# Kernel tuning notes

Measured on AMD Instinct MI355X. Metric: run time of the kernel, lower is better.

Reference implementation:

```python
import jax, jax.numpy as jnp
import numpy as np

B, S = 8, 512
HIDDEN = 513
SPATIAL = HIDDEN - 1           # 512
F = SPATIAL // 2 + 1           # 257 rfft bins
F2, F4 = 2 * F, 4 * F          # 514, 1028
IN_DIM = F2 + F2 + 2 * SPATIAL # 2052
MAX_STEPS = 20
TOL = 1e-3


def _ln(x, g, b):
    m = x.mean(-1, keepdims=True)
    v = ((x - m) ** 2).mean(-1, keepdims=True)
    return (x - m) * jax.lax.rsqrt(v + 1e-5) * g + b


def _freq_net(x, w1, b1, g, beta, w2, b2):
    # Linear -> LayerNorm -> GELU(exact) -> Linear -> Tanh
    h = jax.nn.gelu(_ln(x @ w1 + b1, g, beta), approximate=False)
    return jnp.tanh(h @ w2 + b2)


def _mlp(x, w1, b1, w2, b2):
    # Linear -> GELU(exact) -> Linear
    return jax.nn.gelu(x @ w1 + b1, approximate=False) @ w2 + b2


def setup_inputs() -> dict:
    key = jax.random.key(0)
    ks = jax.random.split(key, 16)
    def n(k, shape, s=0.05):
        return jax.random.normal(k, shape, jnp.float32) * s
    return dict(
        carrier_in=n(ks[0], (B, S, SPATIAL), 1.0),
        trajectory_in=n(ks[1], (B, S, SPATIAL), 1.0),
        source_pos=n(ks[2], (B, HIDDEN), 1.0),
        target_pos=n(ks[3], (B, HIDDEN), 1.0),
        cw1=n(ks[4], (IN_DIM, F4)), cb1=jnp.zeros(F4), cg=jnp.ones(F4), cbeta=jnp.zeros(F4),
        cw2=n(ks[5], (F4, F2)), cb2=jnp.zeros(F2),
        tw1=n(ks[6], (IN_DIM, F4)), tb1=jnp.zeros(F4), tg=jnp.ones(F4), tbeta=jnp.zeros(F4),
        tw2=n(ks[7], (F4, F2)), tb2=jnp.zeros(F2),
        freq_damping=jnp.linspace(0.95, 0.5, F).astype(jnp.float32),
        dw1=n(ks[8], (F2, F)), db1=jnp.zeros(F), dw2=n(ks[9], (F, 1)), db2=jnp.ones(1),
        sw1=n(ks[10], (F2, F // 2)), sb1=jnp.zeros(F // 2), sw2=n(ks[11], (F // 2, 1)), sb2=jnp.ones(1),
        carrier_scale=jnp.float32(0.1), trajectory_scale=jnp.float32(0.1),
    )


def reference(carrier_in, trajectory_in, source_pos, target_pos,
              cw1, cb1, cg, cbeta, cw2, cb2,
              tw1, tb1, tg, tbeta, tw2, tb2,
              freq_damping, dw1, db1, dw2, db2,
              sw1, sb1, sw2, sb2,
              carrier_scale, trajectory_scale):
    b, s, _ = carrier_in.shape
    src = jnp.broadcast_to(source_pos[:, None, :SPATIAL], (b, s, SPATIAL))
    tgt = jnp.broadcast_to(target_pos[:, None, :SPATIAL], (b, s, SPATIAL))

    def to_flat(x):  # rfft -> view_as_real -> flatten: [b,s,2F] (re,im interleaved)
        f = jnp.fft.rfft(x, axis=-1)
        return jnp.stack([f.real, f.imag], axis=-1).reshape(b, s, F2).astype(jnp.float32)

    c0 = to_flat(carrier_in)
    t0 = to_flat(trajectory_in)
    # torch: repeat(1,1,2).flatten -> tiled [d_0..d_{F-1}, d_0..d_{F-1}]
    damping = jnp.concatenate([freq_damping, freq_damping])

    def clamp10(x):
        nrm = jnp.linalg.norm(x)
        return jnp.where(nrm > 10.0, x * (10.0 / nrm), x)

    def step(carry, _):
        c, t, done = carry
        combined = jnp.concatenate([c, t, src, tgt], axis=-1)  # [b,s,IN_DIM]
        fc = _freq_net(combined, cw1, cb1, cg, cbeta, cw2, cb2)
        ft = _freq_net(combined, tw1, tb1, tg, tbeta, tw2, tb2)
        safe_c = jnp.nan_to_num(c, nan=0.0, posinf=1e6, neginf=-1e6)
        safe_t = jnp.nan_to_num(t, nan=0.0, posinf=1e6, neginf=-1e6)
        alpha_c = jax.nn.sigmoid(_mlp(safe_c, dw1, db1, dw2, db2))
        alpha_t = jax.nn.sigmoid(_mlp(safe_t, dw1, db1, dw2, db2))
        gamma = jax.nn.sigmoid(_mlp(safe_c, sw1, sb1, sw2, sb2)) + 0.5
        alpha_c = jnp.where(jnp.isnan(alpha_c), 0.0, alpha_c)
        alpha_t = jnp.where(jnp.isnan(alpha_t), 0.0, alpha_t)
        new_c = damping * c + gamma * alpha_c * carrier_scale * fc
        new_t = damping * t + gamma * alpha_t * trajectory_scale * ft
        dc = jnp.linalg.norm(new_c - c, axis=-1).mean()
        dt = jnp.linalg.norm(new_t - t, axis=-1).mean()
        conv = (dc < TOL) & (dt < TOL)
        # on convergence the torch loop breaks BEFORE the norm clamp
        out_c = jnp.where(conv, new_c, clamp10(new_c))
        out_t = jnp.where(conv, new_t, clamp10(new_t))
        out_c = jnp.where(done, c, out_c)
        out_t = jnp.where(done, t, out_t)
        return (out_c, out_t, done | conv), None

    (cf, tf, _), _ = jax.lax.scan(step, (c0, t0, jnp.array(False)), None, length=MAX_STEPS)

    def to_spatial(x):
        xr = x.reshape(b, s, F, 2)
        return jnp.fft.irfft(xr[..., 0] + 1j * xr[..., 1], n=SPATIAL, axis=-1).astype(jnp.float32)

    return to_spatial(cf), to_spatial(tf)


if __name__ == '__main__':
    out = reference(**setup_inputs())
    print(out[0].shape, out[1].shape)
```

## Files before the change

kernel.cpp:

```cpp
#include <hip/hip_runtime.h>
#include <hip/hip_bf16.h>
#include <math.h>

typedef __hip_bfloat16 bf16;
using s16x8 = __attribute__((ext_vector_type(8))) short;
using f32x4 = __attribute__((ext_vector_type(4))) float;
typedef __attribute__((address_space(1))) const unsigned int gu32;
typedef __attribute__((address_space(3))) unsigned int lu32;

#define RTOT 4096
#define XCT  1056
#define NT1  2176
#define HLD  2176
#define KH   1088
#define CLD  640
#define KDP  576
#define NDC  512
#define F2E  514
#define SP   512
#define YZS  16

__device__ __forceinline__ float gelu_ex(float x) {
    return 0.5f * x * (1.0f + erff(x * 0.70710678118654752f));
}
__device__ __forceinline__ float sigm(float x) { return 1.0f / (1.0f + expf(-x)); }
__device__ __forceinline__ float n2n(float x) {
    if (isnan(x)) return 0.0f;
    if (isinf(x)) return x > 0.0f ? 1e6f : -1e6f;
    return x;
}
__device__ __forceinline__ unsigned short bfb(float x) {
    __hip_bfloat16 h = __float2bfloat16(x);
    return *(unsigned short*)&h;
}
__device__ __forceinline__ unsigned packbf(float x, float y) {
    return (unsigned)bfb(x) | ((unsigned)bfb(y) << 16);
}
__device__ __forceinline__ void glds16(const bf16* g, short* l) {
    __builtin_amdgcn_global_load_lds((gu32*)g, (lu32*)l, 16, 0, 0);
}

template<int EPI, int BNT>
__global__ __launch_bounds__(256)
void gemm_bt(const bf16* __restrict__ A, int lda,
             const bf16* __restrict__ Bt, int ldb,
             float* __restrict__ C, int ldc,
             const float* __restrict__ bias, int bias_ld, int ktiles,
             long zA, long zB, long zC, long zBias)
{
    A    += (long)blockIdx.z * zA;
    Bt   += (long)blockIdx.z * zB;
    C    += (long)blockIdx.z * zC;
    bias += (long)blockIdx.z * zBias;

    constexpr int NC = BNT / 32;
    __shared__ __align__(16) short As[2][128 * 32];
    __shared__ __align__(16) short Bs[2][BNT * 32];
    const int tid  = threadIdx.x;
    const int lane = tid & 63;
    const int wave = tid >> 6;
    const int l15  = lane & 15, kl = lane >> 4;
    const long mb = (long)blockIdx.x * 128;
    const long nb = (long)blockIdx.y * BNT;
    const int wr = (wave >> 1) * 64;
    const int wc = (wave & 1) * (BNT / 2);

    f32x4 acc[4][NC] = {};

    const int grp_r = lane >> 2;
    const int gcol  = (lane & 3) * 8;
    const bf16* gA0 = A  + (mb + wave * 32 + grp_r) * (long)lda + gcol;
    const bf16* gA1 = gA0 + 16 * (long)lda;
    const int brow0 = (BNT == 128) ? wave * 32 : wave * 16;
    const bf16* gB0 = Bt + (nb + brow0 + grp_r) * (long)ldb + gcol;
    const bf16* gB1 = gB0 + 16 * (long)ldb;

    auto stage = [&](int buf, int kt) {
        const long ko = (long)kt * 32;
        glds16(gA0 + ko, &As[buf][(wave * 32) * 32]);
        glds16(gA1 + ko, &As[buf][(wave * 32 + 16) * 32]);
        glds16(gB0 + ko, &Bs[buf][brow0 * 32]);
        if (BNT == 128) glds16(gB1 + ko, &Bs[buf][(brow0 + 16) * 32]);
    };

    stage(0, 0);
    __syncthreads();
    int cur = 0;
    for (int kt = 0; kt < ktiles; ++kt) {
        if (kt + 1 < ktiles) stage(cur ^ 1, kt + 1);
        s16x8 af[4], bfr[NC];
#pragma unroll
        for (int m = 0; m < 4; ++m) {
            int ar = wr + m * 16 + l15;
            af[m] = *reinterpret_cast<const s16x8*>(&As[cur][ar * 32 + kl * 8]);
        }
#pragma unroll
        for (int n = 0; n < NC; ++n) {
            int br = wc + n * 16 + l15;
            bfr[n] = *reinterpret_cast<const s16x8*>(&Bs[cur][br * 32 + kl * 8]);
        }
#pragma unroll
        for (int m = 0; m < 4; ++m)
#pragma unroll
            for (int n = 0; n < NC; ++n)
                acc[m][n] = __builtin_amdgcn_mfma_f32_16x16x32_bf16(af[m], bfr[n], acc[m][n], 0, 0, 0);
        __syncthreads();
        cur ^= 1;
    }

    const float* brow = bias + (bias_ld ? (long)(mb >> 9) * bias_ld : 0);
#pragma unroll
    for (int m = 0; m < 4; ++m) {
        const long grow0 = mb + wr + m * 16 + kl * 4;
#pragma unroll
        for (int n = 0; n < NC; ++n) {
            const long gcol2 = nb + wc + n * 16 + l15;
            const float bb = brow[gcol2];
            f32x4 v = acc[m][n];
#pragma unroll
            for (int r = 0; r < 4; ++r) {
                float x = v[r] + bb;
                if (EPI == 1) x = tanhf(x);
                else if (EPI == 2) x = gelu_ex(x);
                C[(grow0 + r) * (long)ldc + gcol2] = x;
            }
        }
    }
}

__global__ __launch_bounds__(256)
void sgemm_bt(const float* __restrict__ A, int lda,
              const float* __restrict__ Bt, int ldb,
              float* __restrict__ C, int ldc, int ktiles)
{
    __shared__ float As[16][68];
    __shared__ float Bs[16][68];
    const int tid = threadIdx.x;
    const int tx = tid & 15, ty = tid >> 4;
    const int lr = tid >> 2, lc = (tid & 3) * 4;
    const long mb = (long)blockIdx.x * 64, nb = (long)blockIdx.y * 64;
    float acc[4][4] = {};
    const float* Ap = A  + (mb + lr) * (long)lda + lc;
    const float* Bp = Bt + (nb + lr) * (long)ldb + lc;
    for (int kt = 0; kt < ktiles; ++kt) {
        float4 av = *(const float4*)(Ap + kt * 16);
        float4 bv = *(const float4*)(Bp + kt * 16);
        __syncthreads();
        As[lc + 0][lr] = av.x; As[lc + 1][lr] = av.y;
        As[lc + 2][lr] = av.z; As[lc + 3][lr] = av.w;
        Bs[lc + 0][lr] = bv.x; Bs[lc + 1][lr] = bv.y;
        Bs[lc + 2][lr] = bv.z; Bs[lc + 3][lr] = bv.w;
        __syncthreads();
#pragma unroll
        for (int kk = 0; kk < 16; ++kk) {
            float4 a = *(const float4*)&As[kk][ty * 4];
            float4 b = *(const float4*)&Bs[kk][tx * 4];
            acc[0][0] = fmaf(a.x, b.x, acc[0][0]); acc[0][1] = fmaf(a.x, b.y, acc[0][1]);
            acc[0][2] = fmaf(a.x, b.z, acc[0][2]); acc[0][3] = fmaf(a.x, b.w, acc[0][3]);
            acc[1][0] = fmaf(a.y, b.x, acc[1][0]); acc[1][1] = fmaf(a.y, b.y, acc[1][1]);
            acc[1][2] = fmaf(a.y, b.z, acc[1][2]); acc[1][3] = fmaf(a.y, b.w, acc[1][3]);
            acc[2][0] = fmaf(a.z, b.x, acc[2][0]); acc[2][1] = fmaf(a.z, b.y, acc[2][1]);
            acc[2][2] = fmaf(a.z, b.z, acc[2][2]); acc[2][3] = fmaf(a.z, b.w, acc[2][3]);
            acc[3][0] = fmaf(a.w, b.x, acc[3][0]); acc[3][1] = fmaf(a.w, b.y, acc[3][1]);
            acc[3][2] = fmaf(a.w, b.z, acc[3][2]); acc[3][3] = fmaf(a.w, b.w, acc[3][3]);
        }
    }
#pragma unroll
    for (int i = 0; i < 4; ++i) {
        float4 st = { acc[i][0], acc[i][1], acc[i][2], acc[i][3] };
        *(float4*)&C[(mb + ty * 4 + i) * (long)ldc + nb + tx * 4] = st;
    }
}

__global__ void build_tables(float* __restrict__ RT, float* __restrict__ IT)
{
    long idx = (long)blockIdx.x * 256 + threadIdx.x;
    const double W = 6.283185307179586476925286766559005768 / 512.0;
    if (idx < 640L * 512) {
        int r = (int)(idx >> 9), n = (int)(idx & 511);
        float v = 0.f;
        if (r < F2E) {
            int bin = r >> 1;
            int m = (bin * n) & 511;
            double ang = W * m;
            v = (r & 1) ? (float)(-sin(ang)) : (float)cos(ang);
        }
        RT[idx] = v;
    } else {
        long j2 = idx - 640L * 512;
        if (j2 < 512L * 640) {
            int n = (int)(j2 / 640), j = (int)(j2 % 640);
            float v = 0.f;
            if (j < F2E) {
                int bin = j >> 1;
                int m = (bin * n) & 511;
                double ang = W * m;
                bool edge = (bin == 0 || bin == 256);
                double ck = edge ? 1.0 : 2.0;
                if (j & 1) v = edge ? 0.f : (float)(-ck * sin(ang) / 512.0);
                else       v = (float)(ck * cos(ang) / 512.0);
            }
            IT[j2] = v;
        }
    }
}

__global__ void build_damp(float* damp, const float* __restrict__ fd)
{
    int i = blockIdx.x * 256 + threadIdx.x;
    if (i < F2E) damp[i] = fd[i < 257 ? i : i - 257];
}

__global__ void ybase_part(const float* __restrict__ srcp, const float* __restrict__ tgtp,
                           const float* __restrict__ cw1, const float* __restrict__ tw1,
                           float* __restrict__ Yp)
{
    const int n = blockIdx.x * 256 + threadIdx.x;
    const int b = blockIdx.y, z = blockIdx.z;
    if (n >= NT1) return;
    float acc = 0.f;
    if (n < 2056) {
        const bool isT = (n >= 1028);
        const int nn = isT ? n - 1028 : n;
        const float* w = isT ? tw1 : cw1;
        const float* s = srcp + b * 513;
        const float* t = tgtp + b * 513;
        const int k0 = z * (512 / YZS);
        for (int k = k0; k < k0 + 512 / YZS; ++k) {
            acc = fmaf(s[k], w[(size_t)(1028 + k) * 1028 + nn], acc);
            acc = fmaf(t[k], w[(size_t)(1540 + k) * 1028 + nn], acc);
        }
    }
    Yp[((size_t)z * 8 + b) * NT1 + n] = acc;
}

__global__ void ybase_reduce(const float* __restrict__ Yp,
                             const float* __restrict__ cb1, const float* __restrict__ tb1,
                             float* __restrict__ Yb)
{
    const int n = blockIdx.x * 256 + threadIdx.x;
    const int b = blockIdx.y;
    if (n >= NT1) return;
    float acc = 0.f;
    if (n < 2056) acc = (n < 1028) ? cb1[n] : tb1[n - 1028];
    for (int z = 0; z < YZS; ++z) acc += Yp[((size_t)z * 8 + b) * NT1 + n];
    Yb[b * NT1 + n] = acc;
}

__global__ void wprep(bf16* __restrict__ dst, int ldk,
                      const float* s0, int K0, int N0, int r00,
                      const float* s1, int K1, int N1, int r01)
{
    int r = blockIdx.x;
    int k = blockIdx.y * 256 + threadIdx.x;
    if (k >= ldk) return;
    float v = 0.f;
    if (s0 && r >= r00 && r < r00 + N0 && k < K0) v = s0[(long)k * N0 + (r - r00)];
    if (s1 && r >= r01 && r < r01 + N1 && k < K1) v = s1[(long)k * N1 + (r - r01)];
    dst[(long)r * ldk + k] = __float2bfloat16(v);
}

__global__ void bias_fill(float* __restrict__ dst, int n,
                          const float* s0, int l0, int o0,
                          const float* s1, int l1, int o1)
{
    int i = blockIdx.x * 256 + threadIdx.x;
    if (i >= n) return;
    float v = 0.f;
    if (s0 && i >= o0 && i < o0 + l0) v = s0[i - o0];
    if (s1 && i >= o1 && i < o1 + l1) v = s1[i - o1];
    dst[i] = v;
}

__global__ void initconv(const float* __restrict__ cb, const float* __restrict__ tb,
                         bf16* __restrict__ X, bf16* __restrict__ Cb, bf16* __restrict__ Tb)
{
    int row = blockIdx.x;
    for (int j = threadIdx.x; j < F2E; j += 256) {
        float cv = cb[(long)row * CLD + j], tv = tb[(long)row * CLD + j];
        X[(long)row * XCT + j]        = __float2bfloat16(cv);
        X[(long)row * XCT + 514 + j]  = __float2bfloat16(tv);
        Cb[(long)row * KDP + j] = __float2bfloat16(n2n(cv));
        Tb[(long)row * KDP + j] = __float2bfloat16(n2n(tv));
    }
}

__global__ void xpad_zero(bf16* __restrict__ X)
{
    int row = blockIdx.x;
    int j = 1028 + threadIdx.x;
    if (j < XCT) X[(long)row * XCT + j] = __float2bfloat16(0.f);
}

__global__ __launch_bounds__(256)
void ln_gelu(const float* __restrict__ Y, bf16* __restrict__ H,
             const float* __restrict__ cg, const float* __restrict__ cbeta,
             const float* __restrict__ tg, const float* __restrict__ tbeta)
{
    const int lane = threadIdx.x & 63, wave = threadIdx.x >> 6;
    const int p = blockIdx.x * 4 + wave;
    const int row = p >> 1, net = p & 1;
    const float4* y4 = (const float4*)(Y + (long)row * NT1 + net * 1028);
    float4 v[4], vt = {0.f, 0.f, 0.f, 0.f};
    float s = 0.f;
#pragma unroll
    for (int k = 0; k < 4; ++k) {
        v[k] = y4[lane + k * 64];
        s += v[k].x + v[k].y + v[k].z + v[k].w;
    }
    if (lane == 0) { vt = y4[256]; s += vt.x + vt.y + vt.z + vt.w; }
#pragma unroll
    for (int o = 1; o < 64; o <<= 1) s += __shfl_xor(s, o, 64);
    const float mean = s * (1.0f / 1028.0f);
    float vs = 0.f;
#pragma unroll
    for (int k = 0; k < 4; ++k) {
        float a = v[k].x - mean, b = v[k].y - mean, c = v[k].z - mean, d = v[k].w - mean;
        vs += a * a + b * b + c * c + d * d;
    }
    if (lane == 0) {
        float a = vt.x - mean, b = vt.y - mean, c = vt.z - mean, d = vt.w - mean;
        vs += a * a + b * b + c * c + d * d;
    }
#pragma unroll
    for (int o = 1; o < 64; o <<= 1) vs += __shfl_xor(vs, o, 64);
    const float rs = rsqrtf(vs * (1.0f / 1028.0f) + 1e-5f);
    const float4* g4 = (const float4*)(net ? tg : cg);
    const float4* b4 = (const float4*)(net ? tbeta : cbeta);
    bf16* h = H + (long)row * HLD + (long)net * KH;
#pragma unroll
    for (int k = 0; k < 4; ++k) {
        int j = lane + k * 64;
        float4 gv = g4[j], bv = b4[j];
        ushort4 o;
        o.x = bfb(gelu_ex((v[k].x - mean) * rs * gv.x + bv.x));
        o.y = bfb(gelu_ex((v[k].y - mean) * rs * gv.y + bv.y));
        o.z = bfb(gelu_ex((v[k].z - mean) * rs * gv.z + bv.z));
        o.w = bfb(gelu_ex((v[k].w - mean) * rs * gv.w + bv.w));
        *(ushort4*)(&h[j * 4]) = o;
    }
    if (lane == 0) {
        float4 gv = g4[256], bv = b4[256];
        ushort4 o;
        o.x = bfb(gelu_ex((vt.x - mean) * rs * gv.x + bv.x));
        o.y = bfb(gelu_ex((vt.y - mean) * rs * gv.y + bv.y));
        o.z = bfb(gelu_ex((vt.z - mean) * rs * gv.z + bv.z));
        o.w = bfb(gelu_ex((vt.w - mean) * rs * gv.w + bv.w));
        *(ushort4*)(&h[1024]) = o;
    }
}

__global__ __launch_bounds__(256)
void fused_update(const float* __restrict__ Hd,
                  const float* __restrict__ dw2, const float* __restrict__ db2,
                  const float* __restrict__ sw2, const float* __restrict__ sb2,
                  const float* __restrict__ c, const float* __restrict__ t,
                  const float* __restrict__ fc, const float* __restrict__ ft,
                  float* __restrict__ nc, float* __restrict__ nt,
                  const float* __restrict__ damp,
                  const float* __restrict__ csc, const float* __restrict__ tsc,
                  float* __restrict__ part)
{
    __shared__ float red[16];
    const int tid = threadIdx.x, lane = tid & 63, wave = tid >> 6;
    const int row = blockIdx.x * 4 + wave;

    const float* hc = Hd + (long)row * NDC;
    const float* ht = Hd + (long)(4096 + row) * NDC;
    float s1 = 0.f, s2 = 0.f, s3 = 0.f;
#pragma unroll
    for (int k = 0; k < 4; ++k) {
        int j = lane + k * 64;
        s1 += hc[j] * dw2[j];
        s3 += ht[j] * dw2[j];
    }
    if (lane == 0) { s1 += hc[256] * dw2[256]; s3 += ht[256] * dw2[256]; }
#pragma unroll
    for (int k = 0; k < 2; ++k) {
        int j = lane + k * 64;
        s2 += hc[257 + j] * sw2[j];
    }
#pragma unroll
    for (int o = 1; o < 64; o <<= 1) {
        s1 += __shfl_xor(s1, o, 64);
        s2 += __shfl_xor(s2, o, 64);
        s3 += __shfl_xor(s3, o, 64);
    }
    float a  = sigm(s1 + db2[0]);
    float at = sigm(s3 + db2[0]);
    float g  = sigm(s2 + sb2[0]) + 0.5f;
    if (isnan(a))  a  = 0.f;
    if (isnan(at)) at = 0.f;
    const float gac = g * a  * csc[0];
    const float gat = g * at * tsc[0];

    const float2* c2  = (const float2*)(c  + (long)row * CLD);
    const float2* t2  = (const float2*)(t  + (long)row * CLD);
    const float2* fc2 = (const float2*)(fc + (long)row * CLD);
    const float2* ft2 = (const float2*)(ft + (long)row * CLD);
    float2* nc2 = (float2*)(nc + (long)row * CLD);
    float2* nt2 = (float2*)(nt + (long)row * CLD);
    const float2* d2 = (const float2*)damp;
    float sdc = 0.f, snc = 0.f, sdt = 0.f, snt = 0.f;
#pragma unroll
    for (int k = 0; k < 4; ++k) {
        int j = lane + k * 64;
        float2 dv = d2[j];
        float2 cv = c2[j], fv = fc2[j];
        float2 ncv = { dv.x * cv.x + gac * fv.x, dv.y * cv.y + gac * fv.y };
        nc2[j] = ncv;
        float dx = ncv.x - cv.x, dy = ncv.y - cv.y;
        sdc += dx * dx + dy * dy;
        snc += ncv.x * ncv.x + ncv.y * ncv.y;
        float2 tv = t2[j], gv = ft2[j];
        float2 ntv = { dv.x * tv.x + gat * gv.x, dv.y * tv.y + gat * gv.y };
        nt2[j] = ntv;
        dx = ntv.x - tv.x; dy = ntv.y - tv.y;
        sdt += dx * dx + dy * dy;
        snt += ntv.x * ntv.x + ntv.y * ntv.y;
    }
    if (lane == 0) {
        float2 dv = d2[256];
        float2 cv = c2[256], fv = fc2[256];
        float2 ncv = { dv.x * cv.x + gac * fv.x, dv.y * cv.y + gac * fv.y };
        nc2[256] = ncv;
        float dx = ncv.x - cv.x, dy = ncv.y - cv.y;
        sdc += dx * dx + dy * dy;
        snc += ncv.x * ncv.x + ncv.y * ncv.y;
        float2 tv = t2[256], gv = ft2[256];
        float2 ntv = { dv.x * tv.x + gat * gv.x, dv.y * tv.y + gat * gv.y };
        nt2[256] = ntv;
        dx = ntv.x - tv.x; dy = ntv.y - tv.y;
        sdt += dx * dx + dy * dy;
        snt += ntv.x * ntv.x + ntv.y * ntv.y;
    }
#pragma unroll
    for (int o = 1; o < 64; o <<= 1) {
        sdc += __shfl_xor(sdc, o, 64);
        snc += __shfl_xor(snc, o, 64);
        sdt += __shfl_xor(sdt, o, 64);
        snt += __shfl_xor(snt, o, 64);
    }
    if (lane == 0) {
        red[wave * 4 + 0] = sqrtf(sdc);
        red[wave * 4 + 1] = sqrtf(sdt);
        red[wave * 4 + 2] = snc;
        red[wave * 4 + 3] = snt;
    }
    __syncthreads();
    if (tid < 4)
        part[tid * 1024 + blockIdx.x] =
            red[0 * 4 + tid] + red[1 * 4 + tid] + red[2 * 4 + tid] + red[3 * 4 + tid];
}

__global__ __launch_bounds__(256)
void update3(float* __restrict__ c, float* __restrict__ t,
             const float* __restrict__ nc, const float* __restrict__ nt,
             bf16* __restrict__ X, bf16* __restrict__ Cb, bf16* __restrict__ Tb,
             const float* __restrict__ part, float* __restrict__ scal, int step)
{
    __shared__ float red[4];
    const int tid = threadIdx.x, lane = tid & 63, wave = tid >> 6;
    {
        const float* pq = part + wave * 1024;
        float s = 0.f;
#pragma unroll
        for (int k = 0; k < 16; ++k) s += pq[lane + k * 64];
#pragma unroll
        for (int o = 1; o < 64; o <<= 1) s += __shfl_xor(s, o, 64);
        if (lane == 0) red[wave] = s;
    }
    __syncthreads();
    const float done = scal[step];
    const float dc = red[0] * (1.0f / 4096.0f);
    const float dt = red[1] * (1.0f / 4096.0f);
    const bool conv = (dc < 1e-3f) && (dt < 1e-3f);
    if (blockIdx.x == 0 && tid == 0)
        scal[step + 1] = (done != 0.f || conv) ? 1.f : 0.f;
    if (done != 0.f) return;
    const float nrc = sqrtf(red[2]);
    const float nrt = sqrtf(red[3]);
    const float sc = conv ? 1.f : (nrc > 10.f ? 10.f / nrc : 1.f);
    const float st = conv ? 1.f : (nrt > 10.f ? 10.f / nrt : 1.f);

    const int row = blockIdx.x * 4 + wave;
    const float2* nc2 = (const float2*)(nc + (long)row * CLD);
    const float2* nt2 = (const float2*)(nt + (long)row * CLD);
    float2* c2 = (float2*)(c + (long)row * CLD);
    float2* t2 = (float2*)(t + (long)row * CLD);
    bf16* xr = X  + (long)row * XCT;
    bf16* cb = Cb + (long)row * KDP;
    bf16* tb = Tb + (long)row * KDP;
#pragma unroll
    for (int k = 0; k < 5; ++k) {
        int j = lane + k * 64;
        if (k == 4 && lane > 0) break;
        float2 cv = nc2[j]; cv.x *= sc; cv.y *= sc;
        float2 tv = nt2[j]; tv.x *= st; tv.y *= st;
        c2[j] = cv;
        t2[j] = tv;
        *(unsigned*)(xr + j * 2)       = packbf(cv.x, cv.y);
        *(unsigned*)(xr + 514 + j * 2) = packbf(tv.x, tv.y);
        *(unsigned*)(cb + j * 2) = packbf(n2n(cv.x), n2n(cv.y));
        *(unsigned*)(tb + j * 2) = packbf(n2n(tv.x), n2n(tv.y));
    }
}

extern "C" void kernel_launch(void* const* d_in, const int* in_sizes, int n_in,
                              void* d_out, int out_size, void* d_ws, size_t ws_size,
                              hipStream_t stream)
{
    (void)in_sizes; (void)n_in; (void)out_size; (void)ws_size;
    const float* carrier = (const float*)d_in[0];
    const float* traj    = (const float*)d_in[1];
    const float* srcp    = (const float*)d_in[2];
    const float* tgtp    = (const float*)d_in[3];
    const float* cw1 = (const float*)d_in[4];  const float* cb1 = (const float*)d_in[5];
    const float* cg  = (const float*)d_in[6];  const float* cbe = (const float*)d_in[7];
    const float* cw2 = (const float*)d_in[8];  const float* cb2 = (const float*)d_in[9];
    const float* tw1 = (const float*)d_in[10]; const float* tb1 = (const float*)d_in[11];
    const float* tg  = (const float*)d_in[12]; const float* tbe = (const float*)d_in[13];
    const float* tw2 = (const float*)d_in[14]; const float* tb2 = (const float*)d_in[15];
    const float* fd  = (const float*)d_in[16];
    const float* dw1 = (const float*)d_in[17]; const float* db1 = (const float*)d_in[18];
    const float* dw2 = (const float*)d_in[19]; const float* db2 = (const float*)d_in[20];
    const float* sw1 = (const float*)d_in[21]; const float* sb1 = (const float*)d_in[22];
    const float* sw2 = (const float*)d_in[23]; const float* sb2 = (const float*)d_in[24];
    const float* csc = (const float*)d_in[25]; const float* tsc = (const float*)d_in[26];

    char* p = (char*)d_ws;
    size_t off = 0;
    auto take = [&](size_t bytes) { size_t o = off; off += (bytes + 255) & ~(size_t)255; return o; };
    bf16*  Xct  = (bf16*) (p + take((size_t)RTOT * XCT * 2));
    bf16*  W1ct = (bf16*) (p + take((size_t)NT1 * XCT * 2));
    float* Y    = (float*)(p + take((size_t)RTOT * NT1 * 4));
    bf16*  H    = (bf16*) (p + take((size_t)RTOT * HLD * 2));
    bf16*  W2t  = (bf16*) (p + take((size_t)1280 * KH * 2));
    bf16*  Wdc  = (bf16*) (p + take((size_t)NDC * KDP * 2));
    float* Ybase= (float*)(p + take((size_t)8 * NT1 * 4));
    float* Ypart= (float*)(p + take((size_t)YZS * 8 * NT1 * 4));
    float* b2c  = (float*)(p + take(1280 * 4));
    float* bdc  = (float*)(p + take(NDC * 4));
    float* RT   = (float*)(p + take(640L * 512 * 4));
    float* IT   = (float*)(p + take(512L * 640 * 4));
    float* damp = (float*)(p + take(F2E * 4));
    float* cbuf = (float*)(p + take((size_t)RTOT * CLD * 4));
    float* tbuf = (float*)(p + take((size_t)RTOT * CLD * 4));
    float* ncb  = (float*)(p + take((size_t)RTOT * CLD * 4));
    float* ntb  = (float*)(p + take((size_t)RTOT * CLD * 4));
    float* fcb  = (float*)(p + take((size_t)2 * RTOT * CLD * 4));
    float* ftb  = fcb + (size_t)RTOT * CLD;
    bf16*  Cbb  = (bf16*) (p + take((size_t)2 * RTOT * KDP * 2));
    bf16*  Tbb  = Cbb + (size_t)RTOT * KDP;
    float* Hd   = (float*)(p + take((size_t)2 * RTOT * NDC * 4));
    float* part = (float*)(p + take(4096 * 4));
    float* scal = (float*)(p + take(1024));

    hipMemsetAsync(scal, 0, 1024, stream);

    build_tables<<<2560, 256, 0, stream>>>(RT, IT);
    build_damp<<<3, 256, 0, stream>>>(damp, fd);
    ybase_part<<<dim3(9, 8, YZS), 256, 0, stream>>>(srcp, tgtp, cw1, tw1, Ypart);
    ybase_reduce<<<dim3(9, 8), 256, 0, stream>>>(Ypart, cb1, tb1, Ybase);
    wprep<<<dim3(NT1, 5), 256, 0, stream>>>(W1ct, XCT, cw1, 1028, 1028, 0, tw1, 1028, 1028, 1028);
    wprep<<<dim3(1280, 5), 256, 0, stream>>>(W2t, KH, cw2, 1028, 514, 0, tw2, 1028, 514, 640);
    wprep<<<dim3(NDC, 3), 256, 0, stream>>>(Wdc, KDP, dw1, 514, 257, 0, sw1, 514, 128, 257);
    bias_fill<<<5, 256, 0, stream>>>(b2c, 1280, cb2, 514, 0, tb2, 514, 640);
    bias_fill<<<2, 256, 0, stream>>>(bdc, NDC, db1, 257, 0, sb1, 128, 257);
    xpad_zero<<<RTOT, 32, 0, stream>>>(Xct);

    sgemm_bt<<<dim3(64, 10), 256, 0, stream>>>(carrier, SP, RT, SP, cbuf, CLD, 32);
    sgemm_bt<<<dim3(64, 10), 256, 0, stream>>>(traj,    SP, RT, SP, tbuf, CLD, 32);
    initconv<<<RTOT, 256, 0, stream>>>(cbuf, tbuf, Xct, Cbb, Tbb);

    for (int s = 0; s < 20; ++s) {
        gemm_bt<0, 128><<<dim3(32, 17), 256, 0, stream>>>(Xct, XCT, W1ct, XCT, Y, NT1,
                                                          Ybase, NT1, 33, 0, 0, 0, 0);
        ln_gelu<<<2048, 256, 0, stream>>>(Y, H, cg, cbe, tg, tbe);
        gemm_bt<1, 64><<<dim3(32, 10, 2), 256, 0, stream>>>(H, HLD, W2t, KH, fcb, CLD,
                                                            b2c, 0, 34,
                                                            (long)KH, (long)640 * KH,
                                                            (long)RTOT * CLD, 640);
        gemm_bt<2, 64><<<dim3(64, 8), 256, 0, stream>>>(Cbb, KDP, Wdc, KDP, Hd, NDC,
                                                        bdc, 0, 18, 0, 0, 0, 0);
        fused_update<<<1024, 256, 0, stream>>>(Hd, dw2, db2, sw2, sb2,
                                               cbuf, tbuf, fcb, ftb, ncb, ntb,
                                               damp, csc, tsc, part);
        update3<<<1024, 256, 0, stream>>>(cbuf, tbuf, ncb, ntb, Xct, Cbb, Tbb,
                                          part, scal, s);
    }

    float* out = (float*)d_out;
    sgemm_bt<<<dim3(64, 8), 256, 0, stream>>>(cbuf, CLD, IT, CLD, out, SP, 40);
    sgemm_bt<<<dim3(64, 8), 256, 0, stream>>>(tbuf, CLD, IT, CLD, out + (size_t)RTOT * SP, SP, 40);
}
```

Before: 2.692 ms.

## Share X buffer for damping/step GEMM and drop separate Cb/Tb copies

Repacks the X activation so the trajectory half starts at an aligned offset (528), letting the damping/step GEMM read carrier and trajectory directly from X via z-strides instead of separate sanitized bf16 copies. This removes the Cb/Tb writes in update3 and initconv along with the NaN/Inf sanitisation, and W1 is re-laid out to match the padded K. The first GEMM's tile width also changes from 128 to 64 columns, doubling the grid. The risk is that NaN/Inf inputs to the damping net are no longer sanitized before the GEMM, and the narrower tiles reuse data less.

```diff
diff --git a/kernel.cpp b/kernel.cpp
--- a/kernel.cpp
+++ b/kernel.cpp
@@ -10,12 +10,13 @@
 
 #define RTOT 4096
 #define XCT  1056
+#define TOFF 528
 #define NT1  2176
 #define HLD  2176
 #define KH   1088
 #define CLD  640
+#define NDC  512
 #define KDP  576
-#define NDC  512
 #define F2E  514
 #define SP   512
 #define YZS  16
@@ -24,11 +25,6 @@
     return 0.5f * x * (1.0f + erff(x * 0.70710678118654752f));
 }
 __device__ __forceinline__ float sigm(float x) { return 1.0f / (1.0f + expf(-x)); }
-__device__ __forceinline__ float n2n(float x) {
-    if (isnan(x)) return 0.0f;
-    if (isinf(x)) return x > 0.0f ? 1e6f : -1e6f;
-    return x;
-}
 __device__ __forceinline__ unsigned short bfb(float x) {
     __hip_bfloat16 h = __float2bfloat16(x);
     return *(unsigned short*)&h;
@@ -247,6 +243,24 @@
     Yb[b * NT1 + n] = acc;
 }
 
+__global__ void w1prep(bf16* __restrict__ dst,
+                       const float* __restrict__ cw1, const float* __restrict__ tw1)
+{
+    const int r = blockIdx.x;
+    const int k = blockIdx.y * 256 + threadIdx.x;
+    if (k >= XCT) return;
+    float v = 0.f;
+    if (r < 2056) {
+        const float* w = (r < 1028) ? cw1 : tw1;
+        const int nn = (r < 1028) ? r : r - 1028;
+        int kk = -1;
+        if (k < 514) kk = k;
+        else if (k >= TOFF && k < TOFF + 514) kk = 514 + (k - TOFF);
+        if (kk >= 0) v = w[(size_t)kk * 1028 + nn];
+    }
+    dst[(long)r * XCT + k] = __float2bfloat16(v);
+}
+
 __global__ void wprep(bf16* __restrict__ dst, int ldk,
                       const float* s0, int K0, int N0, int r00,
                       const float* s1, int K1, int N1, int r01)
@@ -273,23 +287,23 @@
 }
 
 __global__ void initconv(const float* __restrict__ cb, const float* __restrict__ tb,
-                         bf16* __restrict__ X, bf16* __restrict__ Cb, bf16* __restrict__ Tb)
+                         bf16* __restrict__ X)
 {
     int row = blockIdx.x;
     for (int j = threadIdx.x; j < F2E; j += 256) {
-        float cv = cb[(long)row * CLD + j], tv = tb[(long)row * CLD + j];
-        X[(long)row * XCT + j]        = __float2bfloat16(cv);
-        X[(long)row * XCT + 514 + j]  = __float2bfloat16(tv);
-        Cb[(long)row * KDP + j] = __float2bfloat16(n2n(cv));
-        Tb[(long)row * KDP + j] = __float2bfloat16(n2n(tv));
+        X[(long)row * XCT + j]        = __float2bfloat16(cb[(long)row * CLD + j]);
+        X[(long)row * XCT + TOFF + j] = __float2bfloat16(tb[(long)row * CLD + j]);
     }
 }
 
 __global__ void xpad_zero(bf16* __restrict__ X)
 {
     int row = blockIdx.x;
-    int j = 1028 + threadIdx.x;
-    if (j < XCT) X[(long)row * XCT + j] = __float2bfloat16(0.f);
+    int t = threadIdx.x;
+    if (t < 28) {
+        int j = (t < 14) ? (514 + t) : (TOFF + 514 + (t - 14));
+        X[(long)row * XCT + j] = __float2bfloat16(0.f);
+    }
 }
 
 __global__ __launch_bounds__(256)
@@ -456,7 +470,7 @@
 __global__ __launch_bounds__(256)
 void update3(float* __restrict__ c, float* __restrict__ t,
              const float* __restrict__ nc, const float* __restrict__ nt,
-             bf16* __restrict__ X, bf16* __restrict__ Cb, bf16* __restrict__ Tb,
+             bf16* __restrict__ X,
              const float* __restrict__ part, float* __restrict__ scal, int step)
 {
     __shared__ float red[4];
@@ -488,9 +502,7 @@
     const float2* nt2 = (const float2*)(nt + (long)row * CLD);
     float2* c2 = (float2*)(c + (long)row * CLD);
     float2* t2 = (float2*)(t + (long)row * CLD);
-    bf16* xr = X  + (long)row * XCT;
-    bf16* cb = Cb + (long)row * KDP;
-    bf16* tb = Tb + (long)row * KDP;
+    bf16* xr = X + (long)row * XCT;
 #pragma unroll
     for (int k = 0; k < 5; ++k) {
         int j = lane + k * 64;
@@ -499,10 +511,8 @@
         float2 tv = nt2[j]; tv.x *= st; tv.y *= st;
         c2[j] = cv;
         t2[j] = tv;
-        *(unsigned*)(xr + j * 2)       = packbf(cv.x, cv.y);
-        *(unsigned*)(xr + 514 + j * 2) = packbf(tv.x, tv.y);
-        *(unsigned*)(cb + j * 2) = packbf(n2n(cv.x), n2n(cv.y));
-        *(unsigned*)(tb + j * 2) = packbf(n2n(tv.x), n2n(tv.y));
+        *(unsigned*)(xr + j * 2)        = packbf(cv.x, cv.y);
+        *(unsigned*)(xr + TOFF + j * 2) = packbf(tv.x, tv.y);
     }
 }
 
@@ -550,8 +560,6 @@
     float* ntb  = (float*)(p + take((size_t)RTOT * CLD * 4));
     float* fcb  = (float*)(p + take((size_t)2 * RTOT * CLD * 4));
     float* ftb  = fcb + (size_t)RTOT * CLD;
-    bf16*  Cbb  = (bf16*) (p + take((size_t)2 * RTOT * KDP * 2));
-    bf16*  Tbb  = Cbb + (size_t)RTOT * KDP;
     float* Hd   = (float*)(p + take((size_t)2 * RTOT * NDC * 4));
     float* part = (float*)(p + take(4096 * 4));
     float* scal = (float*)(p + take(1024));
@@ -562,7 +570,7 @@
     build_damp<<<3, 256, 0, stream>>>(damp, fd);
     ybase_part<<<dim3(9, 8, YZS), 256, 0, stream>>>(srcp, tgtp, cw1, tw1, Ypart);
     ybase_reduce<<<dim3(9, 8), 256, 0, stream>>>(Ypart, cb1, tb1, Ybase);
-    wprep<<<dim3(NT1, 5), 256, 0, stream>>>(W1ct, XCT, cw1, 1028, 1028, 0, tw1, 1028, 1028, 1028);
+    w1prep<<<dim3(NT1, 5), 256, 0, stream>>>(W1ct, cw1, tw1);
     wprep<<<dim3(1280, 5), 256, 0, stream>>>(W2t, KH, cw2, 1028, 514, 0, tw2, 1028, 514, 640);
     wprep<<<dim3(NDC, 3), 256, 0, stream>>>(Wdc, KDP, dw1, 514, 257, 0, sw1, 514, 128, 257);
     bias_fill<<<5, 256, 0, stream>>>(b2c, 1280, cb2, 514, 0, tb2, 514, 640);
@@ -571,23 +579,24 @@
 
     sgemm_bt<<<dim3(64, 10), 256, 0, stream>>>(carrier, SP, RT, SP, cbuf, CLD, 32);
     sgemm_bt<<<dim3(64, 10), 256, 0, stream>>>(traj,    SP, RT, SP, tbuf, CLD, 32);
-    initconv<<<RTOT, 256, 0, stream>>>(cbuf, tbuf, Xct, Cbb, Tbb);
+    initconv<<<RTOT, 256, 0, stream>>>(cbuf, tbuf, Xct);
 
     for (int s = 0; s < 20; ++s) {
-        gemm_bt<0, 128><<<dim3(32, 17), 256, 0, stream>>>(Xct, XCT, W1ct, XCT, Y, NT1,
-                                                          Ybase, NT1, 33, 0, 0, 0, 0);
+        gemm_bt<0, 64><<<dim3(32, 34), 256, 0, stream>>>(Xct, XCT, W1ct, XCT, Y, NT1,
+                                                         Ybase, NT1, 33, 0, 0, 0, 0);
         ln_gelu<<<2048, 256, 0, stream>>>(Y, H, cg, cbe, tg, tbe);
         gemm_bt<1, 64><<<dim3(32, 10, 2), 256, 0, stream>>>(H, HLD, W2t, KH, fcb, CLD,
                                                             b2c, 0, 34,
                                                             (long)KH, (long)640 * KH,
                                                             (long)RTOT * CLD, 640);
-        gemm_bt<2, 64><<<dim3(64, 8), 256, 0, stream>>>(Cbb, KDP, Wdc, KDP, Hd, NDC,
-                                                        bdc, 0, 18, 0, 0, 0, 0);
+        gemm_bt<2, 64><<<dim3(32, 8, 2), 256, 0, stream>>>(Xct, XCT, Wdc, KDP, Hd, NDC,
+                                                           bdc, 0, 18,
+                                                           (long)TOFF, 0,
+                                                           (long)RTOT * NDC, 0);
         fused_update<<<1024, 256, 0, stream>>>(Hd, dw2, db2, sw2, sb2,
                                                cbuf, tbuf, fcb, ftb, ncb, ntb,
                                                damp, csc, tsc, part);
-        update3<<<1024, 256, 0, stream>>>(cbuf, tbuf, ncb, ntb, Xct, Cbb, Tbb,
-                                          part, scal, s);
+        update3<<<1024, 256, 0, stream>>>(cbuf, tbuf, ncb, ntb, Xct, part, scal, s);
     }
 
     float* out = (float*)d_out;
```

Result: no change. 2.735 ms (+1.6%).
